# Kernel optimization log

Hardware: AMD Instinct MI355X
Metric: run time of the kernel (lower is better)

Reference implementation:

```python
import jax, jax.numpy as jnp
import numpy as np

LINHAS, COLUNAS, DIM, BATCH = 32, 32, 256, 2048
NEURONS = LINHAS * COLUNAS
TAXA_INICIAL = 0.5
SIGMA_INICIAL = max(LINHAS, COLUNAS) / 2.0  # 16.0


def _grid_locs():
    # matches tf.meshgrid default 'xy' indexing, stacked then flattened
    x = jnp.arange(LINHAS, dtype=jnp.float32)
    y = jnp.arange(COLUNAS, dtype=jnp.float32)
    g = jnp.stack(jnp.meshgrid(x, y), axis=-1)  # (COLUNAS, LINHAS, 2)
    return g.reshape(-1, 2)


def setup_inputs() -> dict:
    key = jax.random.key(0)
    k1, k2 = jax.random.split(key)
    X = jax.random.normal(k1, (BATCH, DIM), dtype=jnp.float32)
    # keras 'random_normal' initializer: stddev 0.05
    pesos = jax.random.normal(k2, (NEURONS, DIM), dtype=jnp.float32) * 0.05
    return {
        "X": X,
        "pesos": pesos,
        "localizacoes": _grid_locs(),
        "passo_atual": 100,
        "total_passos": 1000,
    }


def reference(X, pesos, localizacoes, passo_atual, total_passos):
    frac = jnp.float32(passo_atual) / jnp.float32(total_passos)
    taxa = TAXA_INICIAL * jnp.exp(-frac)
    sigma = SIGMA_INICIAL * jnp.exp(-frac)

    # squared-euclidean distances (B, N)
    x2 = jnp.sum(X * X, axis=1, keepdims=True)
    w2 = jnp.sum(pesos * pesos, axis=1)
    dist = x2 + w2 - 2.0 * (X @ pesos.T)

    bmu_idx = jnp.argmin(dist, axis=1)            # (B,)
    bmu_loc = localizacoes[bmu_idx]               # (B, 2)

    # grid distances and Gaussian neighborhood (B, N)
    dist_grade = jnp.sum((localizacoes[None, :, :] - bmu_loc[:, None, :]) ** 2, axis=2)
    h = jnp.exp(-dist_grade / (2.0 * sigma ** 2))

    # delta_total = mean_b taxa * h[b,n] * (X[b,d] - W[n,d]), computed without
    # materializing the (B, N, D) tensor:
    B = jnp.float32(X.shape[0])
    delta_total = taxa * (jnp.einsum('bn,bd->nd', h, X) - jnp.sum(h, axis=0)[:, None] * pesos) / B

    new_pesos = pesos + delta_total
    return new_pesos
```

## Files before the change

### kernel.cpp

```cpp
#include <hip/hip_runtime.h>
#include <float.h>

#define Bsz 2048
#define Nn  1024
#define Dd  256

typedef __attribute__((ext_vector_type(8))) short bf16x8;
typedef __attribute__((ext_vector_type(4))) float f32x4;
typedef unsigned long long u64;

__device__ __forceinline__ unsigned short bfr(float x) {
    unsigned u = __float_as_uint(x);
    u += 0x7fffu + ((u >> 16) & 1u);
    return (unsigned short)(u >> 16);
}
__device__ __forceinline__ float bf2f(unsigned short h) {
    return __uint_as_float(((unsigned)h) << 16);
}

__device__ __forceinline__ void som_params(const int* __restrict__ step,
                                           const int* __restrict__ total,
                                           float* taxa, float* inv2s2) {
    float frac = (float)(*step) / (float)(*total);
    float e = __expf(-frac);
    *taxa = 0.5f * e;
    float sigma = 16.0f * e;
    *inv2s2 = 1.0f / (2.0f * sigma * sigma);
}

__device__ __forceinline__ u64 packsc(float f, int n) {
    unsigned u = __float_as_uint(f);
    u = (u & 0x80000000u) ? ~u : (u | 0x80000000u);
    return ((u64)u << 32) | (unsigned)n;
}

__global__ __launch_bounds__(256) void prep_all(
    const float* __restrict__ X, const float* __restrict__ W,
    ushort* __restrict__ Xhi, ushort* __restrict__ Xlo,
    ushort* __restrict__ Whi, ushort* __restrict__ Wlo,
    ushort* __restrict__ Xt, float* __restrict__ w2,
    u64* __restrict__ bmin)
{
    __shared__ float ld[64][65];
    const int t = threadIdx.x;
    const int bid = blockIdx.x;

    if (bid < 256) {
        int row  = bid * 4 + (t >> 6);
        int lane = t & 63;
        float4 v = ((const float4*)(W + (size_t)row * Dd))[lane];
        float s = v.x*v.x + v.y*v.y + v.z*v.z + v.w*v.w;
        #pragma unroll
        for (int m = 32; m; m >>= 1) s += __shfl_xor(s, m, 64);
        if (lane == 0) w2[row] = s;
        ushort4 h4, l4;
        h4.x = bfr(v.x); l4.x = bfr(v.x - bf2f(h4.x));
        h4.y = bfr(v.y); l4.y = bfr(v.y - bf2f(h4.y));
        h4.z = bfr(v.z); l4.z = bfr(v.z - bf2f(h4.z));
        h4.w = bfr(v.w); l4.w = bfr(v.w - bf2f(h4.w));
        *(ushort4*)&Whi[(size_t)row * Dd + lane * 4] = h4;
        *(ushort4*)&Wlo[(size_t)row * Dd + lane * 4] = l4;
    } else {
        const int idx = bid - 256;
        const int b0 = (idx & 31) * 64;
        const int d0 = (idx >> 5) * 64;

        if ((idx >> 5) == 0 && t < 64) bmin[b0 + t] = ~0ull;

        #pragma unroll
        for (int p = 0; p < 4; ++p) {
            int flat = p * 256 + t;
            int row = flat >> 4, c4 = flat & 15;
            float4 v = *(const float4*)&X[(size_t)(b0 + row) * Dd + d0 + c4 * 4];
            ushort4 h4, l4;
            h4.x = bfr(v.x); l4.x = bfr(v.x - bf2f(h4.x));
            h4.y = bfr(v.y); l4.y = bfr(v.y - bf2f(h4.y));
            h4.z = bfr(v.z); l4.z = bfr(v.z - bf2f(h4.z));
            h4.w = bfr(v.w); l4.w = bfr(v.w - bf2f(h4.w));
            size_t off = (size_t)(b0 + row) * Dd + d0 + c4 * 4;
            *(ushort4*)&Xhi[off] = h4;
            *(ushort4*)&Xlo[off] = l4;
            ld[row][c4*4+0] = v.x; ld[row][c4*4+1] = v.y;
            ld[row][c4*4+2] = v.z; ld[row][c4*4+3] = v.w;
        }
        __syncthreads();
        #pragma unroll
        for (int q = 0; q < 2; ++q) {
            int idx2 = q * 256 + t;
            int d  = idx2 >> 3;
            int bs = (idx2 & 7) * 8;
            bf16x8 o;
            #pragma unroll
            for (int j = 0; j < 8; ++j) o[j] = (short)bfr(ld[bs + j][d]);
            *(bf16x8*)&Xt[(size_t)(d0 + d) * Bsz + b0 + bs] = o;
        }
    }
}

__global__ __launch_bounds__(256) void bmu_mfma(
    const ushort* __restrict__ Xhi, const ushort* __restrict__ Xlo,
    const ushort* __restrict__ Whi, const ushort* __restrict__ Wlo,
    const float* __restrict__ w2, u64* __restrict__ bmin)
{
    const int t = threadIdx.x, w = t >> 6, l = t & 63;
    const int wm = w & 1, wn = w >> 1;
    const int b0 = blockIdx.x * 128 + wm * 64;
    const int n0 = blockIdx.y * 64 + wn * 32;
    const int lr = l & 15, lg = l >> 4;

    f32x4 acc[4][2];
    #pragma unroll
    for (int m = 0; m < 4; ++m)
        #pragma unroll
        for (int n = 0; n < 2; ++n) { f32x4 z = {0.f,0.f,0.f,0.f}; acc[m][n] = z; }

    #pragma unroll
    for (int kd = 0; kd < Dd; kd += 32) {
        bf16x8 ah[4], al[4], bh[2], bl[2];
        #pragma unroll
        for (int m = 0; m < 4; ++m) {
            size_t off = (size_t)(b0 + m*16 + lr) * Dd + kd + lg*8;
            ah[m] = *(const bf16x8*)&Xhi[off];
            al[m] = *(const bf16x8*)&Xlo[off];
        }
        #pragma unroll
        for (int n = 0; n < 2; ++n) {
            size_t off = (size_t)(n0 + n*16 + lr) * Dd + kd + lg*8;
            bh[n] = *(const bf16x8*)&Whi[off];
            bl[n] = *(const bf16x8*)&Wlo[off];
        }
        #pragma unroll
        for (int m = 0; m < 4; ++m)
            #pragma unroll
            for (int n = 0; n < 2; ++n) {
                acc[m][n] = __builtin_amdgcn_mfma_f32_16x16x32_bf16(ah[m], bh[n], acc[m][n], 0, 0, 0);
                acc[m][n] = __builtin_amdgcn_mfma_f32_16x16x32_bf16(ah[m], bl[n], acc[m][n], 0, 0, 0);
                acc[m][n] = __builtin_amdgcn_mfma_f32_16x16x32_bf16(al[m], bh[n], acc[m][n], 0, 0, 0);
            }
    }

    float w2v[2]; int nidx[2];
    #pragma unroll
    for (int n = 0; n < 2; ++n) { nidx[n] = n0 + n*16 + lr; w2v[n] = w2[nidx[n]]; }

    #pragma unroll
    for (int m = 0; m < 4; ++m)
        #pragma unroll
        for (int r = 0; r < 4; ++r) {
            u64 p0 = packsc(w2v[0] - 2.f * acc[m][0][r], nidx[0]);
            u64 p1 = packsc(w2v[1] - 2.f * acc[m][1][r], nidx[1]);
            u64 pm = p1 < p0 ? p1 : p0;
            #pragma unroll
            for (int msk = 1; msk < 16; msk <<= 1) {
                unsigned plo = (unsigned)pm, phi = (unsigned)(pm >> 32);
                plo = __shfl_xor(plo, msk, 64);
                phi = __shfl_xor(phi, msk, 64);
                u64 o = ((u64)phi << 32) | plo;
                if (o < pm) pm = o;
            }
            if (lr == 0) {
                int b = b0 + m*16 + lg*4 + r;
                atomicMin(&bmin[b], pm);
            }
        }
}

__global__ __launch_bounds__(512) void acc_finish(
    const ushort* __restrict__ Xt, const u64* __restrict__ bmin,
    const float* __restrict__ W, const int* __restrict__ step,
    const int* __restrict__ total, float* __restrict__ out)
{
    __shared__ float red[8][32][36];
    __shared__ float hws[8][32];

    const int t = threadIdx.x, w = t >> 6, l = t & 63;
    const int lr = l & 15, lg = l >> 4;
    const int n0 = blockIdx.x * 32;
    const int d0 = blockIdx.y * 32;

    float taxa, inv2s2;
    som_params(step, total, &taxa, &inv2s2);

    const float fny  = (float)(n0 >> 5);
    const float fnx0 = (float)lr;
    const float fnx1 = (float)(lr + 16);

    f32x4 acc[2][2];
    #pragma unroll
    for (int m = 0; m < 2; ++m)
        #pragma unroll
        for (int nf = 0; nf < 2; ++nf) { f32x4 z = {0.f,0.f,0.f,0.f}; acc[m][nf] = z; }
    float hs0 = 0.f, hs1 = 0.f;

    #pragma unroll
    for (int ks = 0; ks < 8; ++ks) {
        const int bk = w * 256 + ks * 32 + lg * 8;
        bf16x8 am0, am1;
        #pragma unroll
        for (int j = 0; j < 8; ++j) {
            unsigned idx = (unsigned)(bmin[bk + j] & 0xffffffffu);
            float bx = (float)(idx & 31), by = (float)(idx >> 5);
            float dy  = fny - by;
            float dy2 = dy * dy;
            float dx0 = fnx0 - bx, dx1 = fnx1 - bx;
            float h0 = __expf(-(dx0*dx0 + dy2) * inv2s2);
            float h1 = __expf(-(dx1*dx1 + dy2) * inv2s2);
            am0[j] = (short)bfr(h0);
            am1[j] = (short)bfr(h1);
            hs0 += h0; hs1 += h1;
        }
        bf16x8 bx0 = *(const bf16x8*)&Xt[(size_t)(d0 + lr)      * Bsz + bk];
        bf16x8 bx1 = *(const bf16x8*)&Xt[(size_t)(d0 + 16 + lr) * Bsz + bk];
        acc[0][0] = __builtin_amdgcn_mfma_f32_16x16x32_bf16(am0, bx0, acc[0][0], 0, 0, 0);
        acc[0][1] = __builtin_amdgcn_mfma_f32_16x16x32_bf16(am0, bx1, acc[0][1], 0, 0, 0);
        acc[1][0] = __builtin_amdgcn_mfma_f32_16x16x32_bf16(am1, bx0, acc[1][0], 0, 0, 0);
        acc[1][1] = __builtin_amdgcn_mfma_f32_16x16x32_bf16(am1, bx1, acc[1][1], 0, 0, 0);
    }

    hs0 += __shfl_xor(hs0, 16, 64); hs0 += __shfl_xor(hs0, 32, 64);
    hs1 += __shfl_xor(hs1, 16, 64); hs1 += __shfl_xor(hs1, 32, 64);
    if (l < 16) { hws[w][l] = hs0; hws[w][16 + l] = hs1; }

    #pragma unroll
    for (int m = 0; m < 2; ++m)
        #pragma unroll
        for (int nf = 0; nf < 2; ++nf)
            #pragma unroll
            for (int r = 0; r < 4; ++r)
                red[w][m*16 + lg*4 + r][nf*16 + lr] = acc[m][nf][r];
    __syncthreads();

    const float invB = 1.0f / 2048.0f;
    const int nl = t >> 4;
    const int dl = (t & 15) * 2;
    float s0 = 0.f, s1 = 0.f, hsn = 0.f;
    #pragma unroll
    for (int ww = 0; ww < 8; ++ww) {
        s0  += red[ww][nl][dl];
        s1  += red[ww][nl][dl + 1];
        hsn += hws[ww][nl];
    }
    const int n = n0 + nl;
    const int d = d0 + dl;
    const float* wp = &W[(size_t)n * Dd + d];
    float wv0 = wp[0], wv1 = wp[1];
    float2 o = make_float2(wv0 + taxa * (s0 - hsn * wv0) * invB,
                           wv1 + taxa * (s1 - hsn * wv1) * invB);
    *(float2*)&out[(size_t)n * Dd + d] = o;
}

extern "C" void kernel_launch(void* const* d_in, const int* in_sizes, int n_in,
                              void* d_out, int out_size, void* d_ws, size_t ws_size,
                              hipStream_t stream)
{
    const float* X    = (const float*)d_in[0];
    const float* W    = (const float*)d_in[1];
    const int* step   = (const int*)d_in[3];
    const int* total  = (const int*)d_in[4];
    float* out = (float*)d_out;

    char* p = (char*)d_ws;
    float* w2   = (float*)p;  p += 4096;
    u64*   bmin = (u64*)p;    p += 16384;
    ushort* Xt  = (ushort*)p; p += 1048576;
    ushort* Xhi = (ushort*)p; p += 1048576;
    ushort* Xlo = (ushort*)p; p += 1048576;
    ushort* Whi = (ushort*)p; p += 524288;
    ushort* Wlo = (ushort*)p; p += 524288;

    prep_all  <<<384, 256, 0, stream>>>(X, W, Xhi, Xlo, Whi, Wlo, Xt, w2, bmin);
    bmu_mfma  <<<dim3(16, 16), 256, 0, stream>>>(Xhi, Xlo, Whi, Wlo, w2, bmin);
    acc_finish<<<dim3(32, 8), 512, 0, stream>>>(Xt, bmin, W, step, total, out);
}
```

Baseline: 37.22 us.

## Fuse bf16 split and BMU GEMM into prep kernel, replace atomics with partial minima

The bf16 hi/lo splitting of X and W and the row-norm computation move into the BMU MFMA kernel, so the Xhi/Xlo/Whi/Wlo buffers and one kernel launch go away. Each block writes per-column-tile partial minima instead of doing 64-bit atomicMin, and acc_finish reduces the 16 partials per sample into a shared index table. The BMU blocks now redo the split of X and W redundantly across tiles (more ALU work and fp32 reads). Every acc_finish block also re-reads all 256KB of partials.

```diff
diff --git a/kernel.cpp b/kernel.cpp
--- a/kernel.cpp
+++ b/kernel.cpp
@@ -34,52 +34,107 @@
     return ((u64)u << 32) | (unsigned)n;
 }
 
-__global__ __launch_bounds__(256) void prep_all(
+__device__ __forceinline__ float split8(const float* __restrict__ src,
+                                        bf16x8* hi, bf16x8* lo) {
+    float4 v0 = *(const float4*)src;
+    float4 v1 = *(const float4*)(src + 4);
+    float f[8] = {v0.x, v0.y, v0.z, v0.w, v1.x, v1.y, v1.z, v1.w};
+    float s = 0.f;
+    #pragma unroll
+    for (int j = 0; j < 8; ++j) {
+        unsigned short h = bfr(f[j]);
+        (*hi)[j] = (short)h;
+        (*lo)[j] = (short)bfr(f[j] - bf2f(h));
+        s += f[j] * f[j];
+    }
+    return s;
+}
+
+__global__ __launch_bounds__(256) void fused_pre(
     const float* __restrict__ X, const float* __restrict__ W,
-    ushort* __restrict__ Xhi, ushort* __restrict__ Xlo,
-    ushort* __restrict__ Whi, ushort* __restrict__ Wlo,
-    ushort* __restrict__ Xt, float* __restrict__ w2,
-    u64* __restrict__ bmin)
+    ushort* __restrict__ Xt, u64* __restrict__ ppack)
 {
     __shared__ float ld[64][65];
-    const int t = threadIdx.x;
-    const int bid = blockIdx.x;
+    __shared__ u64 lmin[2][2][64];
+
+    const int t = threadIdx.x, bid = blockIdx.x;
+    const int w = t >> 6, l = t & 63;
+    const int lr = l & 15, lg = l >> 4;
 
     if (bid < 256) {
-        int row  = bid * 4 + (t >> 6);
-        int lane = t & 63;
-        float4 v = ((const float4*)(W + (size_t)row * Dd))[lane];
-        float s = v.x*v.x + v.y*v.y + v.z*v.z + v.w*v.w;
-        #pragma unroll
-        for (int m = 32; m; m >>= 1) s += __shfl_xor(s, m, 64);
-        if (lane == 0) w2[row] = s;
-        ushort4 h4, l4;
-        h4.x = bfr(v.x); l4.x = bfr(v.x - bf2f(h4.x));
-        h4.y = bfr(v.y); l4.y = bfr(v.y - bf2f(h4.y));
-        h4.z = bfr(v.z); l4.z = bfr(v.z - bf2f(h4.z));
-        h4.w = bfr(v.w); l4.w = bfr(v.w - bf2f(h4.w));
-        *(ushort4*)&Whi[(size_t)row * Dd + lane * 4] = h4;
-        *(ushort4*)&Wlo[(size_t)row * Dd + lane * 4] = l4;
+        const int wm = w & 1, wn = w >> 1;
+        const int b0 = (bid >> 4) * 128 + wm * 64;
+        const int n0 = (bid & 15) * 64 + wn * 32;
+
+        f32x4 acc[4][2];
+        #pragma unroll
+        for (int m = 0; m < 4; ++m)
+            #pragma unroll
+            for (int n = 0; n < 2; ++n) { f32x4 z = {0.f,0.f,0.f,0.f}; acc[m][n] = z; }
+        float w2a[2] = {0.f, 0.f};
+
+        #pragma unroll
+        for (int kd = 0; kd < Dd; kd += 32) {
+            bf16x8 ah[4], al[4], bh[2], bl[2];
+            #pragma unroll
+            for (int m = 0; m < 4; ++m)
+                split8(&X[(size_t)(b0 + m*16 + lr) * Dd + kd + lg*8], &ah[m], &al[m]);
+            #pragma unroll
+            for (int nf = 0; nf < 2; ++nf)
+                w2a[nf] += split8(&W[(size_t)(n0 + nf*16 + lr) * Dd + kd + lg*8],
+                                  &bh[nf], &bl[nf]);
+            #pragma unroll
+            for (int m = 0; m < 4; ++m)
+                #pragma unroll
+                for (int nf = 0; nf < 2; ++nf) {
+                    acc[m][nf] = __builtin_amdgcn_mfma_f32_16x16x32_bf16(ah[m], bh[nf], acc[m][nf], 0, 0, 0);
+                    acc[m][nf] = __builtin_amdgcn_mfma_f32_16x16x32_bf16(ah[m], bl[nf], acc[m][nf], 0, 0, 0);
+                    acc[m][nf] = __builtin_amdgcn_mfma_f32_16x16x32_bf16(al[m], bh[nf], acc[m][nf], 0, 0, 0);
+                }
+        }
+
+        #pragma unroll
+        for (int nf = 0; nf < 2; ++nf) {
+            w2a[nf] += __shfl_xor(w2a[nf], 16, 64);
+            w2a[nf] += __shfl_xor(w2a[nf], 32, 64);
+        }
+        const int ni0 = n0 + lr, ni1 = n0 + 16 + lr;
+
+        #pragma unroll
+        for (int m = 0; m < 4; ++m)
+            #pragma unroll
+            for (int r = 0; r < 4; ++r) {
+                u64 p0 = packsc(w2a[0] - 2.f * acc[m][0][r], ni0);
+                u64 p1 = packsc(w2a[1] - 2.f * acc[m][1][r], ni1);
+                u64 pm = p1 < p0 ? p1 : p0;
+                #pragma unroll
+                for (int msk = 1; msk < 16; msk <<= 1) {
+                    unsigned plo = (unsigned)pm, phi = (unsigned)(pm >> 32);
+                    plo = __shfl_xor(plo, msk, 64);
+                    phi = __shfl_xor(phi, msk, 64);
+                    u64 o = ((u64)phi << 32) | plo;
+                    if (o < pm) pm = o;
+                }
+                if (lr == 0) lmin[wm][wn][m*16 + lg*4 + r] = pm;
+            }
+        __syncthreads();
+        if (t < 128) {
+            const int bwm = t >> 6, bb = t & 63;
+            u64 a = lmin[bwm][0][bb], c = lmin[bwm][1][bb];
+            u64 pm = c < a ? c : a;
+            const int b = (bid >> 4) * 128 + bwm * 64 + bb;
+            ppack[(size_t)(bid & 15) * Bsz + b] = pm;
+        }
     } else {
         const int idx = bid - 256;
         const int b0 = (idx & 31) * 64;
         const int d0 = (idx >> 5) * 64;
 
-        if ((idx >> 5) == 0 && t < 64) bmin[b0 + t] = ~0ull;
-
         #pragma unroll
         for (int p = 0; p < 4; ++p) {
             int flat = p * 256 + t;
             int row = flat >> 4, c4 = flat & 15;
             float4 v = *(const float4*)&X[(size_t)(b0 + row) * Dd + d0 + c4 * 4];
-            ushort4 h4, l4;
-            h4.x = bfr(v.x); l4.x = bfr(v.x - bf2f(h4.x));
-            h4.y = bfr(v.y); l4.y = bfr(v.y - bf2f(h4.y));
-            h4.z = bfr(v.z); l4.z = bfr(v.z - bf2f(h4.z));
-            h4.w = bfr(v.w); l4.w = bfr(v.w - bf2f(h4.w));
-            size_t off = (size_t)(b0 + row) * Dd + d0 + c4 * 4;
-            *(ushort4*)&Xhi[off] = h4;
-            *(ushort4*)&Xlo[off] = l4;
             ld[row][c4*4+0] = v.x; ld[row][c4*4+1] = v.y;
             ld[row][c4*4+2] = v.z; ld[row][c4*4+3] = v.w;
         }
@@ -97,87 +152,33 @@
     }
 }
 
-__global__ __launch_bounds__(256) void bmu_mfma(
-    const ushort* __restrict__ Xhi, const ushort* __restrict__ Xlo,
-    const ushort* __restrict__ Whi, const ushort* __restrict__ Wlo,
-    const float* __restrict__ w2, u64* __restrict__ bmin)
-{
-    const int t = threadIdx.x, w = t >> 6, l = t & 63;
-    const int wm = w & 1, wn = w >> 1;
-    const int b0 = blockIdx.x * 128 + wm * 64;
-    const int n0 = blockIdx.y * 64 + wn * 32;
-    const int lr = l & 15, lg = l >> 4;
-
-    f32x4 acc[4][2];
-    #pragma unroll
-    for (int m = 0; m < 4; ++m)
-        #pragma unroll
-        for (int n = 0; n < 2; ++n) { f32x4 z = {0.f,0.f,0.f,0.f}; acc[m][n] = z; }
-
-    #pragma unroll
-    for (int kd = 0; kd < Dd; kd += 32) {
-        bf16x8 ah[4], al[4], bh[2], bl[2];
-        #pragma unroll
-        for (int m = 0; m < 4; ++m) {
-            size_t off = (size_t)(b0 + m*16 + lr) * Dd + kd + lg*8;
-            ah[m] = *(const bf16x8*)&Xhi[off];
-            al[m] = *(const bf16x8*)&Xlo[off];
-        }
-        #pragma unroll
-        for (int n = 0; n < 2; ++n) {
-            size_t off = (size_t)(n0 + n*16 + lr) * Dd + kd + lg*8;
-            bh[n] = *(const bf16x8*)&Whi[off];
-            bl[n] = *(const bf16x8*)&Wlo[off];
-        }
-        #pragma unroll
-        for (int m = 0; m < 4; ++m)
-            #pragma unroll
-            for (int n = 0; n < 2; ++n) {
-                acc[m][n] = __builtin_amdgcn_mfma_f32_16x16x32_bf16(ah[m], bh[n], acc[m][n], 0, 0, 0);
-                acc[m][n] = __builtin_amdgcn_mfma_f32_16x16x32_bf16(ah[m], bl[n], acc[m][n], 0, 0, 0);
-                acc[m][n] = __builtin_amdgcn_mfma_f32_16x16x32_bf16(al[m], bh[n], acc[m][n], 0, 0, 0);
-            }
-    }
-
-    float w2v[2]; int nidx[2];
-    #pragma unroll
-    for (int n = 0; n < 2; ++n) { nidx[n] = n0 + n*16 + lr; w2v[n] = w2[nidx[n]]; }
-
-    #pragma unroll
-    for (int m = 0; m < 4; ++m)
-        #pragma unroll
-        for (int r = 0; r < 4; ++r) {
-            u64 p0 = packsc(w2v[0] - 2.f * acc[m][0][r], nidx[0]);
-            u64 p1 = packsc(w2v[1] - 2.f * acc[m][1][r], nidx[1]);
-            u64 pm = p1 < p0 ? p1 : p0;
-            #pragma unroll
-            for (int msk = 1; msk < 16; msk <<= 1) {
-                unsigned plo = (unsigned)pm, phi = (unsigned)(pm >> 32);
-                plo = __shfl_xor(plo, msk, 64);
-                phi = __shfl_xor(phi, msk, 64);
-                u64 o = ((u64)phi << 32) | plo;
-                if (o < pm) pm = o;
-            }
-            if (lr == 0) {
-                int b = b0 + m*16 + lg*4 + r;
-                atomicMin(&bmin[b], pm);
-            }
-        }
-}
-
 __global__ __launch_bounds__(512) void acc_finish(
-    const ushort* __restrict__ Xt, const u64* __restrict__ bmin,
+    const ushort* __restrict__ Xt, const u64* __restrict__ ppack,
     const float* __restrict__ W, const int* __restrict__ step,
     const int* __restrict__ total, float* __restrict__ out)
 {
     __shared__ float red[8][32][36];
     __shared__ float hws[8][32];
+    __shared__ ushort bidx[Bsz];
 
     const int t = threadIdx.x, w = t >> 6, l = t & 63;
     const int lr = l & 15, lg = l >> 4;
     const int n0 = blockIdx.x * 32;
     const int d0 = blockIdx.y * 32;
 
+    #pragma unroll
+    for (int q = 0; q < 4; ++q) {
+        const int b = q * 512 + t;
+        u64 pm = ppack[b];
+        #pragma unroll
+        for (int g = 1; g < 16; ++g) {
+            u64 c = ppack[(size_t)g * Bsz + b];
+            if (c < pm) pm = c;
+        }
+        bidx[b] = (ushort)(pm & 0xffffu);
+    }
+    __syncthreads();
+
     float taxa, inv2s2;
     som_params(step, total, &taxa, &inv2s2);
 
@@ -198,7 +199,7 @@
         bf16x8 am0, am1;
         #pragma unroll
         for (int j = 0; j < 8; ++j) {
-            unsigned idx = (unsigned)(bmin[bk + j] & 0xffffffffu);
+            unsigned idx = bidx[bk + j];
             float bx = (float)(idx & 31), by = (float)(idx >> 5);
             float dy  = fny - by;
             float dy2 = dy * dy;
@@ -260,15 +261,9 @@
     float* out = (float*)d_out;
 
     char* p = (char*)d_ws;
-    float* w2   = (float*)p;  p += 4096;
-    u64*   bmin = (u64*)p;    p += 16384;
-    ushort* Xt  = (ushort*)p; p += 1048576;
-    ushort* Xhi = (ushort*)p; p += 1048576;
-    ushort* Xlo = (ushort*)p; p += 1048576;
-    ushort* Whi = (ushort*)p; p += 524288;
-    ushort* Wlo = (ushort*)p; p += 524288;
-
-    prep_all  <<<384, 256, 0, stream>>>(X, W, Xhi, Xlo, Whi, Wlo, Xt, w2, bmin);
-    bmu_mfma  <<<dim3(16, 16), 256, 0, stream>>>(Xhi, Xlo, Whi, Wlo, w2, bmin);
-    acc_finish<<<dim3(32, 8), 512, 0, stream>>>(Xt, bmin, W, step, total, out);
-}
+    ushort* Xt   = (ushort*)p; p += 1048576;
+    u64*    ppack = (u64*)p;   p += 262144;
+
+    fused_pre <<<384, 256, 0, stream>>>(X, W, Xt, ppack);
+    acc_finish<<<dim3(32, 8), 512, 0, stream>>>(Xt, ppack, W, step, total, out);
+}
```

After: 36.18 us. 1.03x faster.
